# Performance work log

Measured on AMD Instinct MI355X. Metric: run time of the kernel, lower is better.

## Reference

```python
import jax, jax.numpy as jnp
import numpy as np

ST_HIDDEN = 128
ST_HEADS = 4
ST_LAYERS = 3
RES_SCALE = 1.0
DK = ST_HIDDEN // ST_HEADS


def build_3d_adj(spatial_ei, spatial_ea, n_nodes, window):
    # replicate spatial edges per time slice with node offset t*n_nodes
    offs = (jnp.arange(window) * n_nodes)[None, :, None]  # [1,W,1]
    all_sp_idx = (spatial_ei[:, None, :] + offs).reshape(2, -1)  # [2, W*E]
    all_sp_attr = jnp.tile(spatial_ea, (window, 1))  # [W*E, De]
    # temporal edges t -> t+1 for every node
    src = jnp.arange((window - 1) * n_nodes)
    temp_idx = jnp.stack([src, src + n_nodes], axis=0)  # [2, (W-1)*N]
    temp_attr = jnp.broadcast_to(spatial_ea.mean(axis=0, keepdims=True),
                                 (temp_idx.shape[1], spatial_ea.shape[1]))
    ei = jnp.concatenate([all_sp_idx, temp_idx], axis=1)
    ea = jnp.concatenate([all_sp_attr, temp_attr], axis=0)
    return ei, ea


def seg_softmax(logits, dst, num_nodes):
    # logits [E,H], segment softmax over dst (pyg_softmax)
    m = jax.ops.segment_max(logits, dst, num_segments=num_nodes)  # [N,H]
    ex = jnp.exp(logits - m[dst])
    s = jax.ops.segment_sum(ex, dst, num_segments=num_nodes)
    return ex / (s[dst] + 1e-16)


def layernorm(x, g, b, eps=1e-5):
    mu = x.mean(-1, keepdims=True)
    var = ((x - mu) ** 2).mean(-1, keepdims=True)
    return (x - mu) * jax.lax.rsqrt(var + eps) * g + b


def block(x, ei, ea, qw, qb, kw, kb, vw, vb, fw, fb, ow, ob, ln_g, ln_b):
    B, Nt, _ = x.shape
    H, dk = ST_HEADS, DK
    Q = (x @ qw + qb).reshape(B, Nt, H, dk)
    K = (x @ kw + kb).reshape(B, Nt, H, dk)
    V = (x @ vw + vb).reshape(B, Nt, H, dk)
    src, dst = ei[0], ei[1]
    q_e = Q[:, dst]  # [B,E,H,dk]
    k_e = K[:, src]
    v_e = V[:, src]
    film = ea @ fw + fb  # [E, 2*hidden]
    gamma, beta = jnp.split(film, 2, axis=-1)
    gamma = gamma.reshape(1, -1, H, dk)
    beta = beta.reshape(1, -1, H, dk)
    k_e = k_e * (1.0 + gamma) + beta
    logits = (q_e * k_e).sum(-1) / np.sqrt(dk).astype(np.float32)  # [B,E,H]
    att = jax.vmap(lambda l: seg_softmax(l, dst, Nt))(logits)
    msg = att[..., None] * v_e  # [B,E,H,dk]
    out = jnp.zeros((B, Nt, H, dk), x.dtype).at[:, dst].add(msg)
    y = out.reshape(B, Nt, H * dk) @ ow + ob
    return layernorm(x + y, ln_g, ln_b)


def setup_inputs() -> dict:
    key = jax.random.key(0)
    ks = jax.random.split(key, 12)
    B, W, N, Fin, E, De = 2, 16, 1000, 16, 16000, 8
    H, L = ST_HIDDEN, ST_LAYERS
    g = lambda k, s: jax.random.normal(k, s, jnp.float32) * 0.05
    return {
        "xw": jax.random.normal(ks[0], (B, W, N, Fin), jnp.float32),
        "spatial_ei": jax.random.randint(ks[1], (2, E), 0, N),
        "spatial_ea": jax.random.normal(ks[2], (E, De), jnp.float32),
        "in_w": g(ks[3], (Fin, H)), "in_b": jnp.zeros((H,), jnp.float32),
        "qw": g(ks[4], (L, H, H)), "qb": jnp.zeros((L, H), jnp.float32),
        "kw": g(ks[5], (L, H, H)), "kb": jnp.zeros((L, H), jnp.float32),
        "vw": g(ks[6], (L, H, H)), "vb": jnp.zeros((L, H), jnp.float32),
        "fw": g(ks[7], (L, De, 2 * H)), "fb": jnp.zeros((L, 2 * H), jnp.float32),
        "ow": g(ks[8], (L, H, H)), "ob": jnp.zeros((L, H), jnp.float32),
        "ln_g": jnp.ones((L, H), jnp.float32), "ln_b": jnp.zeros((L, H), jnp.float32),
        "head_w": g(ks[9], (H, 1)), "head_b": jnp.zeros((1,), jnp.float32),
    }


def reference(xw, spatial_ei, spatial_ea, in_w, in_b, qw, qb, kw, kb, vw, vb,
              fw, fb, ow, ob, ln_g, ln_b, head_w, head_b):
    B, W, N, Fin = xw.shape
    ei, ea = build_3d_adj(spatial_ei, spatial_ea, N, W)
    x = xw.reshape(B, W * N, Fin) @ in_w + in_b
    for l in range(ST_LAYERS):
        bx = block(x, ei, ea, qw[l], qb[l], kw[l], kb[l], vw[l], vb[l],
                   fw[l], fb[l], ow[l], ob[l], ln_g[l], ln_b[l])
        x = x + RES_SCALE * (bx - x)
    last = x.reshape(B, W, N, -1)[:, -1]  # [B,N,H]
    return jax.nn.softplus(last @ head_w + head_b).squeeze(-1)  # [B,N]
```

## Files before the change

### kernel.cpp

```cpp
#include <hip/hip_runtime.h>
#include <math.h>

constexpr int B    = 2;
constexpr int W    = 16;
constexpr int N    = 1000;
constexpr int FIN  = 16;
constexpr int E    = 16000;
constexpr int DE   = 8;
constexpr int H    = 128;
constexpr int L    = 3;
constexpr int WL   = 4;
constexpr int W0G  = 12;
constexpr int RPB  = WL * N;
constexpr int ROWS = B * RPB;
constexpr int NMAT = 12;

__device__ __forceinline__ float blockSum128(float v) {
  #pragma unroll
  for (int off = 32; off >= 1; off >>= 1) v += __shfl_xor(v, off);
  __shared__ float s2[2];
  int w = threadIdx.x >> 6;
  __syncthreads();
  if ((threadIdx.x & 63) == 0) s2[w] = v;
  __syncthreads();
  return s2[0] + s2[1];
}

__device__ __forceinline__ float dpp_add_xor1(float x) {
  int y = __builtin_amdgcn_update_dpp(0, __float_as_int(x), 0xB1, 0xF, 0xF, true);
  return x + __int_as_float(y);
}
__device__ __forceinline__ float dpp_add_xor2(float x) {
  int y = __builtin_amdgcn_update_dpp(0, __float_as_int(x), 0x4E, 0xF, 0xF, true);
  return x + __int_as_float(y);
}
__device__ __forceinline__ float headSum32(float p) {
  p = dpp_add_xor1(p);
  p = dpp_add_xor2(p);
  p += __shfl_xor(p, 4);
  p += __shfl_xor(p, 8);
  p += __shfl_xor(p, 16);
  return p;
}
__device__ __forceinline__ float dot4(float4 a, float4 b) {
  return a.x * b.x + a.y * b.y + a.z * b.z + a.w * b.w;
}

__global__ void k_count_scan(const int* __restrict__ ei, int* __restrict__ offs,
                             int* __restrict__ cursor, float* __restrict__ meanea) {
  __shared__ int cnt[N];
  __shared__ int scn[1024];
  int t = threadIdx.x;
  if (t < 8) meanea[t] = 0.f;
  if (t < N) cnt[t] = 0;
  __syncthreads();
  int vals[16];
  int nv = 0;
  for (int e = t; e < E; e += 1024) vals[nv++] = ei[E + e];
  for (int i = 0; i < nv; i++) atomicAdd(&cnt[vals[i]], 1);
  __syncthreads();
  int v = (t < N) ? cnt[t] : 0;
  scn[t] = v;
  __syncthreads();
  for (int st = 1; st < 1024; st <<= 1) {
    int add = (t >= st) ? scn[t - st] : 0;
    __syncthreads();
    scn[t] += add;
    __syncthreads();
  }
  if (t < N) {
    offs[t + 1] = scn[t];
    if (t == 0) offs[0] = 0;
    cursor[t] = scn[t] - v;
  }
}

__global__ void k_prep2(const int* __restrict__ ei, const float* __restrict__ ea,
                        int* __restrict__ cursor, int2* __restrict__ csr,
                        float* __restrict__ meanea,
                        const float* __restrict__ qw, const float* __restrict__ kw,
                        const float* __restrict__ vw, const float* __restrict__ ow,
                        float4* __restrict__ wTp4,
                        const float* __restrict__ xw, const float* __restrict__ in_w,
                        const float* __restrict__ in_b, float* __restrict__ x) {
  int bid = blockIdx.x;
  int t = threadIdx.x;
  if (bid < 64) {
    int e = bid * 256 + t;
    if (e < E) {
      int src = ei[e];
      int dst = ei[E + e];
      int pos = atomicAdd(&cursor[dst], 1);
      csr[pos] = make_int2(src, e);
    }
  } else if (bid < 128) {
    __shared__ float sbuf[256];
    int d = t & 7, g = t >> 3;
    float s = 0.f;
    for (int e = (bid - 64) * 32 + g; e < E; e += 64 * 32) s += ea[e * DE + d];
    sbuf[t] = s;
    __syncthreads();
    for (int st = 16; st >= 1; st >>= 1) {
      if (g < st) sbuf[g * 8 + d] += sbuf[(g + st) * 8 + d];
      __syncthreads();
    }
    if (g == 0) atomicAdd(&meanea[d], sbuf[d]);
  } else if (bid < 128 + NMAT * 16) {
    int bid2 = bid - 128;
    int mat = bid2 / 16;
    int pair = bid2 % 16;
    int kk4 = pair * 2 + (t >> 7);
    int c = t & 127;
    int l = mat >> 2, mm = mat & 3;
    const float* src = ((mm == 0) ? qw : (mm == 1) ? kw : (mm == 2) ? vw : ow) + (long)l * H * H;
    int k0 = kk4 * 4;
    float4 v4;
    v4.x = src[(k0 + 0) * H + c];
    v4.y = src[(k0 + 1) * H + c];
    v4.z = src[(k0 + 2) * H + c];
    v4.w = src[(k0 + 3) * H + c];
    wTp4[((long)mat * 32 + kk4) * H + c] = v4;
  } else {
    int bi = bid - (128 + NMAT * 16);
    int b = bi / 63, tt = bi % 63;
    int lr0 = tt * 64;
    __shared__ float xwS[64][FIN];
    __shared__ float inS[FIN][H];
    for (int i = t; i < 64 * FIN; i += 256) {
      int r = i >> 4, k = i & 15;
      int lr = lr0 + r;
      float val = 0.f;
      if (lr < RPB) {
        int wl = lr / N, n = lr % N;
        val = xw[(((long)b * W + (W0G + wl)) * N + n) * FIN + k];
      }
      xwS[r][k] = val;
    }
    for (int i = t; i < FIN * H; i += 256) inS[i >> 7][i & 127] = in_w[i];
    __syncthreads();
    #pragma unroll
    for (int qi = 0; qi < 8; qi++) {
      int idx = t + qi * 256;
      int r = idx >> 5, cq = idx & 31;
      int lr = lr0 + r;
      if (lr < RPB) {
        float4 acc = *(const float4*)(in_b + cq * 4);
        #pragma unroll
        for (int k = 0; k < FIN; k++) {
          float xv = xwS[r][k];
          float4 w4 = *(const float4*)(&inS[k][cq * 4]);
          acc.x += xv * w4.x; acc.y += xv * w4.y; acc.z += xv * w4.z; acc.w += xv * w4.w;
        }
        *(float4*)(x + ((long)b * RPB + lr) * H + cq * 4) = acc;
      }
    }
  }
}

__global__ void k_film(const float* __restrict__ ea, const float* __restrict__ fw,
                       const float* __restrict__ fb, const float* __restrict__ meanea,
                       unsigned int* __restrict__ filmh) {
  int e0 = blockIdx.x * 4;
  int t = threadIdx.x;
  float rgw[DE], rbw[DE];
  #pragma unroll
  for (int d = 0; d < DE; d++) {
    rgw[d] = fw[d * 2 * H + t];
    rbw[d] = fw[d * 2 * H + H + t];
  }
  float fbg = fb[t], fbb = fb[H + t];
  for (int e = e0; e < e0 + 4 && e <= E; e++) {
    float a[DE];
    if (e < E) {
      float4 a0 = *(const float4*)(ea + (long)e * DE);
      float4 a1 = *(const float4*)(ea + (long)e * DE + 4);
      a[0] = a0.x; a[1] = a0.y; a[2] = a0.z; a[3] = a0.w;
      a[4] = a1.x; a[5] = a1.y; a[6] = a1.z; a[7] = a1.w;
    } else {
      #pragma unroll
      for (int d = 0; d < DE; d++) a[d] = meanea[d] * (1.0f / E);
    }
    float g = fbg, be = fbb;
    #pragma unroll
    for (int d = 0; d < DE; d++) {
      g  += a[d] * rgw[d];
      be += a[d] * rbw[d];
    }
    unsigned int gb = __float_as_uint(g);
    gb = (gb + 0x7fffu + ((gb >> 16) & 1u)) >> 16;
    unsigned int bb_ = __float_as_uint(be);
    bb_ = (bb_ + 0x7fffu + ((bb_ >> 16) & 1u)) & 0xffff0000u;
    filmh[(long)e * H + t] = gb | bb_;
  }
}

__global__ void k_gemm(const float* __restrict__ X, const float4* __restrict__ wTp4,
                       int matBase,
                       const float* __restrict__ bq, const float* __restrict__ bk,
                       const float* __restrict__ bv,
                       float* __restrict__ Cq, float* __restrict__ Ck, float* __restrict__ Cv,
                       int base, int rows_pb, int tiles) {
  int m = blockIdx.y;
  const float* bm = (m == 0) ? bq : (m == 1) ? bk : bv;
  float* Cm       = (m == 0) ? Cq : (m == 1) ? Ck : Cv;
  const float4* wp = wTp4 + (long)(matBase + m) * 32 * H;
  int bb = blockIdx.x / tiles;
  int tt = blockIdx.x % tiles;
  int lr0 = tt * 32;
  long grow0 = (long)bb * RPB + base + lr0;
  int t = threadIdx.x;
  __shared__ float xs[32][H];
  #pragma unroll
  for (int qi = 0; qi < 4; qi++) {
    int idx = t + qi * 256;
    int r = idx >> 5, c4 = idx & 31;
    float4 v4 = make_float4(0.f, 0.f, 0.f, 0.f);
    if (lr0 + r < rows_pb) v4 = *(const float4*)(X + (grow0 + r) * H + c4 * 4);
    *(float4*)&xs[r][c4 * 4] = v4;
  }
  __syncthreads();
  int cg = t & 31, rg = t >> 5;
  float4 bias4 = *(const float4*)(bm + cg * 4);
  float4 acc0 = bias4, acc1 = bias4, acc2 = bias4, acc3 = bias4;
  #pragma unroll 4
  for (int kk4 = 0; kk4 < 32; kk4++) {
    const float4* wr = wp + kk4 * H + cg * 4;
    float4 w0 = wr[0], w1 = wr[1], w2 = wr[2], w3 = wr[3];
    float4 x0 = *(const float4*)&xs[rg * 4 + 0][kk4 * 4];
    float4 x1 = *(const float4*)&xs[rg * 4 + 1][kk4 * 4];
    float4 x2 = *(const float4*)&xs[rg * 4 + 2][kk4 * 4];
    float4 x3 = *(const float4*)&xs[rg * 4 + 3][kk4 * 4];
    acc0.x += dot4(x0, w0); acc0.y += dot4(x0, w1); acc0.z += dot4(x0, w2); acc0.w += dot4(x0, w3);
    acc1.x += dot4(x1, w0); acc1.y += dot4(x1, w1); acc1.z += dot4(x1, w2); acc1.w += dot4(x1, w3);
    acc2.x += dot4(x2, w0); acc2.y += dot4(x2, w1); acc2.z += dot4(x2, w2); acc2.w += dot4(x2, w3);
    acc3.x += dot4(x3, w0); acc3.y += dot4(x3, w1); acc3.z += dot4(x3, w2); acc3.w += dot4(x3, w3);
  }
  int lrr = lr0 + rg * 4;
  if (lrr + 0 < rows_pb) *(float4*)(Cm + (grow0 + rg * 4 + 0) * H + cg * 4) = acc0;
  if (lrr + 1 < rows_pb) *(float4*)(Cm + (grow0 + rg * 4 + 1) * H + cg * 4) = acc1;
  if (lrr + 2 < rows_pb) *(float4*)(Cm + (grow0 + rg * 4 + 2) * H + cg * 4) = acc2;
  if (lrr + 3 < rows_pb) *(float4*)(Cm + (grow0 + rg * 4 + 3) * H + cg * 4) = acc3;
}

__global__ void k_attn_oln(const float* __restrict__ Qb, const float* __restrict__ Kb,
                           const float* __restrict__ Vb,
                           const unsigned int* __restrict__ filmh,
                           const int* __restrict__ offs, const int2* __restrict__ csr,
                           const float* __restrict__ x, const float4* __restrict__ owp,
                           const float* __restrict__ ob, const float* __restrict__ lng,
                           const float* __restrict__ lnb, float* __restrict__ xo,
                           int out_lo,
                           const float* __restrict__ hw, const float* __restrict__ hb,
                           float* __restrict__ out, int do_head) {
  int tid = threadIdx.x;
  int nwin = WL - out_lo;
  int idx = blockIdx.x;
  int b = idx / (nwin * N);
  int rem = idx % (nwin * N);
  int wl = out_lo + rem / N;
  int n = rem % N;
  long drow = ((long)b * WL + wl) * N + n;
  float q = Qb[drow * H + tid];
  long sbase = ((long)b * WL + wl) * N;
  long trow  = ((long)b * WL + wl - 1) * N + n;
  const float scale = 0.17677669529663687f;
  int i0 = offs[n], i1 = offs[n + 1];

  unsigned int fh = filmh[(long)E * H + tid];
  float g  = __uint_as_float(fh << 16);
  float be = __uint_as_float(fh & 0xffff0000u);
  float kv = Kb[trow * H + tid];
  float vv = Vb[trow * H + tid];
  float p  = q * (kv * (1.f + g) + be);
  float pe = __expf(headSum32(p) * scale);
  float ssum = pe, acc = pe * vv;

  for (int i4 = i0; i4 < i1; i4 += 4) {
    #pragma unroll
    for (int j = 0; j < 4; j++) {
      int i = i4 + j;
      int ic = (i < i1) ? i : (i1 - 1);
      int2 se = csr[ic];
      long srow = sbase + se.x;
      unsigned int f2 = filmh[(long)se.y * H + tid];
      float g2 = __uint_as_float(f2 << 16);
      float b2 = __uint_as_float(f2 & 0xffff0000u);
      float kv2 = Kb[srow * H + tid];
      float vv2 = Vb[srow * H + tid];
      float p2  = q * (kv2 * (1.f + g2) + b2);
      float pe2 = __expf(headSum32(p2) * scale);
      pe2 = (i < i1) ? pe2 : 0.f;
      ssum += pe2;
      acc  += pe2 * vv2;
    }
  }
  float ab = acc / (ssum + 1e-16f);

  __shared__ float sab[H];
  sab[tid] = ab;
  __syncthreads();
  float y = ob[tid];
  #pragma unroll 8
  for (int kk4 = 0; kk4 < 32; kk4++) {
    float4 w4 = owp[kk4 * H + tid];
    float4 a4 = *(const float4*)&sab[kk4 * 4];
    y += dot4(a4, w4);
  }

  float v = x[drow * H + tid] + y;
  float mu = blockSum128(v) * (1.f / H);
  float dv = v - mu;
  float var = blockSum128(dv * dv) * (1.f / H);
  float o = dv * rsqrtf(var + 1e-5f) * lng[tid] + lnb[tid];

  if (!do_head) {
    xo[drow * H + tid] = o;
  } else {
    float hv = o * hw[tid];
    float tot = blockSum128(hv);
    if (tid == 0) {
      float z = tot + hb[0];
      out[b * N + n] = fmaxf(z, 0.f) + log1pf(expf(-fabsf(z)));
    }
  }
}

extern "C" void kernel_launch(void* const* d_in, const int* in_sizes, int n_in,
                              void* d_out, int out_size, void* d_ws, size_t ws_size,
                              hipStream_t stream) {
  const float* xw   = (const float*)d_in[0];
  const int*   ei   = (const int*)d_in[1];
  const float* ea   = (const float*)d_in[2];
  const float* in_w = (const float*)d_in[3];
  const float* in_b = (const float*)d_in[4];
  const float* qw   = (const float*)d_in[5];
  const float* qb   = (const float*)d_in[6];
  const float* kw   = (const float*)d_in[7];
  const float* kb   = (const float*)d_in[8];
  const float* vw   = (const float*)d_in[9];
  const float* vb   = (const float*)d_in[10];
  const float* fw   = (const float*)d_in[11];
  const float* fb   = (const float*)d_in[12];
  const float* ow   = (const float*)d_in[13];
  const float* ob   = (const float*)d_in[14];
  const float* ln_g = (const float*)d_in[15];
  const float* ln_b = (const float*)d_in[16];
  const float* hw   = (const float*)d_in[17];
  const float* hb   = (const float*)d_in[18];
  float* out = (float*)d_out;

  float* ws   = (float*)d_ws;
  float* x    = ws;
  float* x2   = x  + (long)ROWS * H;
  float* Qb   = x2 + (long)ROWS * H;
  float* Kb   = Qb + (long)ROWS * H;
  float* Vb   = Kb + (long)ROWS * H;
  float* wTp  = Vb + (long)ROWS * H;
  unsigned int* filmh = (unsigned int*)(wTp + (long)NMAT * H * H);
  float* meanea = (float*)(filmh + (long)(E + 1) * H);
  int* offs    = (int*)(meanea + 8);
  int* cursor  = offs + N + 1;
  int2* csr    = (int2*)(cursor + N);
  float4* wTp4 = (float4*)wTp;

  k_count_scan<<<1, 1024, 0, stream>>>(ei, offs, cursor, meanea);
  k_prep2<<<128 + NMAT * 16 + 126, 256, 0, stream>>>(
      ei, ea, cursor, csr, meanea, qw, kw, vw, ow, wTp4, xw, in_w, in_b, x);

  float* xa = x;
  float* xb = x2;
  for (int l = 0; l < L; l++) {
    int in_lo = l, out_lo = l + 1;
    k_film<<<(E + 1 + 3) / 4, 128, 0, stream>>>(
        ea, fw + (long)l * DE * 2 * H, fb + (long)l * 2 * H, meanea, filmh);
    int rows_pb = (WL - in_lo) * N;
    int tiles = (rows_pb + 31) / 32;
    k_gemm<<<dim3(B * tiles, 3), 256, 0, stream>>>(
        xa, wTp4, l * 4, qb + (long)l * H, kb + (long)l * H, vb + (long)l * H,
        Qb, Kb, Vb, in_lo * N, rows_pb, tiles);
    int nout = B * (WL - out_lo) * N;
    int last = (l == L - 1) ? 1 : 0;
    k_attn_oln<<<nout, H, 0, stream>>>(
        Qb, Kb, Vb, filmh, offs, csr,
        xa, wTp4 + ((long)l * 4 + 3) * 32 * H, ob + (long)l * H,
        ln_g + (long)l * H, ln_b + (long)l * H, xb, out_lo,
        hw, hb, out, last);
    float* tmp = xa; xa = xb; xb = tmp;
  }
}
```

Measured before the change: 263.5 us.

## Merge prep, film, gemm and CSR fill kernels; pack two nodes per attention block

Folds the count/scan into the prep kernel. Moves FiLM computation and CSR scatter into a combined mid kernel with the QKV GEMM, which cuts the launches per layer from three to two. The attention kernel now handles two destination nodes per 256-thread block, with per-half LayerNorm reductions in shared memory. The CSR fill now runs only in the layer-0 mid kernel, which adds ordering reliance on the prep kernel's cursor. The one-block scan now covers 4 counts per thread.

```diff
diff --git a/kernel.cpp b/kernel.cpp
--- a/kernel.cpp
+++ b/kernel.cpp
@@ -14,18 +14,11 @@
 constexpr int RPB  = WL * N;
 constexpr int ROWS = B * RPB;
 constexpr int NMAT = 12;
-
-__device__ __forceinline__ float blockSum128(float v) {
-  #pragma unroll
-  for (int off = 32; off >= 1; off >>= 1) v += __shfl_xor(v, off);
-  __shared__ float s2[2];
-  int w = threadIdx.x >> 6;
-  __syncthreads();
-  if ((threadIdx.x & 63) == 0) s2[w] = v;
-  __syncthreads();
-  return s2[0] + s2[1];
-}
-
+constexpr int NFILM = (E + 1 + 7) / 8;
+
+__device__ __forceinline__ float dot4(float4 a, float4 b) {
+  return a.x * b.x + a.y * b.y + a.z * b.z + a.w * b.w;
+}
 __device__ __forceinline__ float dpp_add_xor1(float x) {
   int y = __builtin_amdgcn_update_dpp(0, __float_as_int(x), 0xB1, 0xF, 0xF, true);
   return x + __int_as_float(y);
@@ -42,90 +35,89 @@
   p += __shfl_xor(p, 16);
   return p;
 }
-__device__ __forceinline__ float dot4(float4 a, float4 b) {
-  return a.x * b.x + a.y * b.y + a.z * b.z + a.w * b.w;
-}
-
-__global__ void k_count_scan(const int* __restrict__ ei, int* __restrict__ offs,
-                             int* __restrict__ cursor, float* __restrict__ meanea) {
-  __shared__ int cnt[N];
-  __shared__ int scn[1024];
-  int t = threadIdx.x;
-  if (t < 8) meanea[t] = 0.f;
-  if (t < N) cnt[t] = 0;
-  __syncthreads();
-  int vals[16];
-  int nv = 0;
-  for (int e = t; e < E; e += 1024) vals[nv++] = ei[E + e];
-  for (int i = 0; i < nv; i++) atomicAdd(&cnt[vals[i]], 1);
-  __syncthreads();
-  int v = (t < N) ? cnt[t] : 0;
-  scn[t] = v;
-  __syncthreads();
-  for (int st = 1; st < 1024; st <<= 1) {
-    int add = (t >= st) ? scn[t - st] : 0;
-    __syncthreads();
-    scn[t] += add;
-    __syncthreads();
-  }
-  if (t < N) {
-    offs[t + 1] = scn[t];
-    if (t == 0) offs[0] = 0;
-    cursor[t] = scn[t] - v;
-  }
-}
-
-__global__ void k_prep2(const int* __restrict__ ei, const float* __restrict__ ea,
-                        int* __restrict__ cursor, int2* __restrict__ csr,
-                        float* __restrict__ meanea,
-                        const float* __restrict__ qw, const float* __restrict__ kw,
-                        const float* __restrict__ vw, const float* __restrict__ ow,
-                        float4* __restrict__ wTp4,
-                        const float* __restrict__ xw, const float* __restrict__ in_w,
-                        const float* __restrict__ in_b, float* __restrict__ x) {
+
+__global__ void k_prep(const int* __restrict__ ei, const float* __restrict__ ea,
+                       const float* __restrict__ qw, const float* __restrict__ kw,
+                       const float* __restrict__ vw, const float* __restrict__ ow,
+                       float4* __restrict__ wTp4,
+                       const float* __restrict__ xw, const float* __restrict__ in_w,
+                       const float* __restrict__ in_b, float* __restrict__ x,
+                       float* __restrict__ meanea, int* __restrict__ offs,
+                       int* __restrict__ cursor) {
+  __shared__ union {
+    struct { int cnt[1024]; int sT[256]; } sc;
+    struct { float xwS[64][FIN]; float inS[FIN][H]; } ip;
+    float sbuf[256];
+  } sm;
   int bid = blockIdx.x;
   int t = threadIdx.x;
-  if (bid < 64) {
-    int e = bid * 256 + t;
-    if (e < E) {
-      int src = ei[e];
-      int dst = ei[E + e];
-      int pos = atomicAdd(&cursor[dst], 1);
-      csr[pos] = make_int2(src, e);
-    }
-  } else if (bid < 128) {
-    __shared__ float sbuf[256];
+  if (bid == 0) {
+    int* cnt = sm.sc.cnt;
+    for (int i = t; i < 1024; i += 256) cnt[i] = 0;
+    __syncthreads();
+    for (int e0 = t; e0 < E; e0 += 1024) {
+      int v[4];
+      #pragma unroll
+      for (int j = 0; j < 4; j++) {
+        int e = e0 + j * 256;
+        v[j] = (e < E) ? ei[E + e] : -1;
+      }
+      #pragma unroll
+      for (int j = 0; j < 4; j++) if (v[j] >= 0) atomicAdd(&cnt[v[j]], 1);
+    }
+    __syncthreads();
+    int idx0 = t * 4;
+    int c0 = cnt[idx0], c1 = cnt[idx0 + 1], c2 = cnt[idx0 + 2], c3 = cnt[idx0 + 3];
+    int run = c0 + c1 + c2 + c3;
+    int* sT = sm.sc.sT;
+    sT[t] = run;
+    __syncthreads();
+    for (int st = 1; st < 256; st <<= 1) {
+      int add = (t >= st) ? sT[t - st] : 0;
+      __syncthreads();
+      sT[t] += add;
+      __syncthreads();
+    }
+    int pos = sT[t] - run;
+    int cs[4] = {c0, c1, c2, c3};
+    #pragma unroll
+    for (int j = 0; j < 4; j++) {
+      int i = idx0 + j;
+      if (i < N) { offs[i + 1] = pos + cs[j]; cursor[i] = pos; }
+      pos += cs[j];
+    }
+    if (t == 0) offs[0] = 0;
+  } else if (bid < 49) {
+    int u0 = (bid - 1) * 1024;
+    #pragma unroll
+    for (int q = 0; q < 4; q++) {
+      int o = u0 + q * 256 + t;
+      int mat = o >> 12, rem = o & 4095;
+      int kk4 = rem >> 7, c = rem & 127;
+      int l = mat >> 2, mm = mat & 3;
+      const float* src = ((mm == 0) ? qw : (mm == 1) ? kw : (mm == 2) ? vw : ow)
+                         + (long)l * H * H;
+      int k0 = kk4 * 4;
+      float4 v4 = make_float4(src[(k0 + 0) * H + c], src[(k0 + 1) * H + c],
+                              src[(k0 + 2) * H + c], src[(k0 + 3) * H + c]);
+      wTp4[o] = v4;
+    }
+  } else if (bid < 81) {
+    int eb = bid - 49;
     int d = t & 7, g = t >> 3;
     float s = 0.f;
-    for (int e = (bid - 64) * 32 + g; e < E; e += 64 * 32) s += ea[e * DE + d];
-    sbuf[t] = s;
+    for (int e = eb * 32 + g; e < E; e += 32 * 32) s += ea[e * DE + d];
+    sm.sbuf[t] = s;
     __syncthreads();
     for (int st = 16; st >= 1; st >>= 1) {
-      if (g < st) sbuf[g * 8 + d] += sbuf[(g + st) * 8 + d];
+      if (g < st) sm.sbuf[g * 8 + d] += sm.sbuf[(g + st) * 8 + d];
       __syncthreads();
     }
-    if (g == 0) atomicAdd(&meanea[d], sbuf[d]);
-  } else if (bid < 128 + NMAT * 16) {
-    int bid2 = bid - 128;
-    int mat = bid2 / 16;
-    int pair = bid2 % 16;
-    int kk4 = pair * 2 + (t >> 7);
-    int c = t & 127;
-    int l = mat >> 2, mm = mat & 3;
-    const float* src = ((mm == 0) ? qw : (mm == 1) ? kw : (mm == 2) ? vw : ow) + (long)l * H * H;
-    int k0 = kk4 * 4;
-    float4 v4;
-    v4.x = src[(k0 + 0) * H + c];
-    v4.y = src[(k0 + 1) * H + c];
-    v4.z = src[(k0 + 2) * H + c];
-    v4.w = src[(k0 + 3) * H + c];
-    wTp4[((long)mat * 32 + kk4) * H + c] = v4;
+    if (g == 0) atomicAdd(&meanea[d], sm.sbuf[d]);
   } else {
-    int bi = bid - (128 + NMAT * 16);
+    int bi = bid - 81;
     int b = bi / 63, tt = bi % 63;
     int lr0 = tt * 64;
-    __shared__ float xwS[64][FIN];
-    __shared__ float inS[FIN][H];
     for (int i = t; i < 64 * FIN; i += 256) {
       int r = i >> 4, k = i & 15;
       int lr = lr0 + r;
@@ -134,9 +126,9 @@
         int wl = lr / N, n = lr % N;
         val = xw[(((long)b * W + (W0G + wl)) * N + n) * FIN + k];
       }
-      xwS[r][k] = val;
-    }
-    for (int i = t; i < FIN * H; i += 256) inS[i >> 7][i & 127] = in_w[i];
+      sm.ip.xwS[r][k] = val;
+    }
+    for (int i = t; i < FIN * H; i += 256) sm.ip.inS[i >> 7][i & 127] = in_w[i];
     __syncthreads();
     #pragma unroll
     for (int qi = 0; qi < 8; qi++) {
@@ -147,8 +139,8 @@
         float4 acc = *(const float4*)(in_b + cq * 4);
         #pragma unroll
         for (int k = 0; k < FIN; k++) {
-          float xv = xwS[r][k];
-          float4 w4 = *(const float4*)(&inS[k][cq * 4]);
+          float xv = sm.ip.xwS[r][k];
+          float4 w4 = *(const float4*)(&sm.ip.inS[k][cq * 4]);
           acc.x += xv * w4.x; acc.y += xv * w4.y; acc.z += xv * w4.z; acc.w += xv * w4.w;
         }
         *(float4*)(x + ((long)b * RPB + lr) * H + cq * 4) = acc;
@@ -157,89 +149,104 @@
   }
 }
 
-__global__ void k_film(const float* __restrict__ ea, const float* __restrict__ fw,
-                       const float* __restrict__ fb, const float* __restrict__ meanea,
-                       unsigned int* __restrict__ filmh) {
-  int e0 = blockIdx.x * 4;
+__global__ void k_mid(const float* __restrict__ X, const float4* __restrict__ wTp4,
+                      int matBase,
+                      const float* __restrict__ bq, const float* __restrict__ bk,
+                      const float* __restrict__ bv,
+                      float* __restrict__ Cq, float* __restrict__ Ck, float* __restrict__ Cv,
+                      int base, int rows_pb, int tiles, int nG,
+                      const float* __restrict__ ea, const float* __restrict__ fwl,
+                      const float* __restrict__ fbl, const float* __restrict__ meanea,
+                      unsigned int* __restrict__ filmh,
+                      const int* __restrict__ ei, int* __restrict__ cursor,
+                      int2* __restrict__ csr) {
+  __shared__ float xs[32][H];
+  int u = blockIdx.x;
   int t = threadIdx.x;
-  float rgw[DE], rbw[DE];
-  #pragma unroll
-  for (int d = 0; d < DE; d++) {
-    rgw[d] = fw[d * 2 * H + t];
-    rbw[d] = fw[d * 2 * H + H + t];
-  }
-  float fbg = fb[t], fbb = fb[H + t];
-  for (int e = e0; e < e0 + 4 && e <= E; e++) {
-    float a[DE];
+  if (u < nG) {
+    int m = u / (B * tiles);
+    int r2 = u % (B * tiles);
+    int bb = r2 / tiles, tt = r2 % tiles;
+    const float* bm = (m == 0) ? bq : (m == 1) ? bk : bv;
+    float* Cm       = (m == 0) ? Cq : (m == 1) ? Ck : Cv;
+    const float4* wp = wTp4 + (long)(matBase + m) * 32 * H;
+    int lr0 = tt * 32;
+    long grow0 = (long)bb * RPB + base + lr0;
+    #pragma unroll
+    for (int qi = 0; qi < 4; qi++) {
+      int idx = t + qi * 256;
+      int r = idx >> 5, c4 = idx & 31;
+      float4 v4 = make_float4(0.f, 0.f, 0.f, 0.f);
+      if (lr0 + r < rows_pb) v4 = *(const float4*)(X + (grow0 + r) * H + c4 * 4);
+      *(float4*)&xs[r][c4 * 4] = v4;
+    }
+    __syncthreads();
+    int cg = t & 31, rg = t >> 5;
+    float4 bias4 = *(const float4*)(bm + cg * 4);
+    float4 acc0 = bias4, acc1 = bias4, acc2 = bias4, acc3 = bias4;
+    #pragma unroll 4
+    for (int kk4 = 0; kk4 < 32; kk4++) {
+      const float4* wr = wp + kk4 * H + cg * 4;
+      float4 w0 = wr[0], w1 = wr[1], w2 = wr[2], w3 = wr[3];
+      float4 x0 = *(const float4*)&xs[rg * 4 + 0][kk4 * 4];
+      float4 x1 = *(const float4*)&xs[rg * 4 + 1][kk4 * 4];
+      float4 x2 = *(const float4*)&xs[rg * 4 + 2][kk4 * 4];
+      float4 x3 = *(const float4*)&xs[rg * 4 + 3][kk4 * 4];
+      acc0.x += dot4(x0, w0); acc0.y += dot4(x0, w1); acc0.z += dot4(x0, w2); acc0.w += dot4(x0, w3);
+      acc1.x += dot4(x1, w0); acc1.y += dot4(x1, w1); acc1.z += dot4(x1, w2); acc1.w += dot4(x1, w3);
+      acc2.x += dot4(x2, w0); acc2.y += dot4(x2, w1); acc2.z += dot4(x2, w2); acc2.w += dot4(x2, w3);
+      acc3.x += dot4(x3, w0); acc3.y += dot4(x3, w1); acc3.z += dot4(x3, w2); acc3.w += dot4(x3, w3);
+    }
+    int lrr = lr0 + rg * 4;
+    if (lrr + 0 < rows_pb) *(float4*)(Cm + (grow0 + rg * 4 + 0) * H + cg * 4) = acc0;
+    if (lrr + 1 < rows_pb) *(float4*)(Cm + (grow0 + rg * 4 + 1) * H + cg * 4) = acc1;
+    if (lrr + 2 < rows_pb) *(float4*)(Cm + (grow0 + rg * 4 + 2) * H + cg * 4) = acc2;
+    if (lrr + 3 < rows_pb) *(float4*)(Cm + (grow0 + rg * 4 + 3) * H + cg * 4) = acc3;
+  } else if (u < nG + NFILM) {
+    int ru = u - nG;
+    int c = t & 127, g2 = t >> 7;
+    float rgw[DE], rbw[DE];
+    #pragma unroll
+    for (int d = 0; d < DE; d++) {
+      rgw[d] = fwl[d * 2 * H + c];
+      rbw[d] = fwl[d * 2 * H + H + c];
+    }
+    float fbg = fbl[c], fbb = fbl[H + c];
+    int e0 = ru * 8 + g2 * 4;
+    for (int e = e0; e < e0 + 4; e++) {
+      if (e > E) break;
+      float a[DE];
+      if (e < E) {
+        float4 a0 = *(const float4*)(ea + (long)e * DE);
+        float4 a1 = *(const float4*)(ea + (long)e * DE + 4);
+        a[0] = a0.x; a[1] = a0.y; a[2] = a0.z; a[3] = a0.w;
+        a[4] = a1.x; a[5] = a1.y; a[6] = a1.z; a[7] = a1.w;
+      } else {
+        #pragma unroll
+        for (int d = 0; d < DE; d++) a[d] = meanea[d] * (1.0f / E);
+      }
+      float g = fbg, be = fbb;
+      #pragma unroll
+      for (int d = 0; d < DE; d++) {
+        g  += a[d] * rgw[d];
+        be += a[d] * rbw[d];
+      }
+      unsigned int gb = __float_as_uint(g);
+      gb = (gb + 0x7fffu + ((gb >> 16) & 1u)) >> 16;
+      unsigned int bb_ = __float_as_uint(be);
+      bb_ = (bb_ + 0x7fffu + ((bb_ >> 16) & 1u)) & 0xffff0000u;
+      filmh[(long)e * H + c] = gb | bb_;
+    }
+  } else {
+    int f = u - nG - NFILM;
+    int e = f * 256 + t;
     if (e < E) {
-      float4 a0 = *(const float4*)(ea + (long)e * DE);
-      float4 a1 = *(const float4*)(ea + (long)e * DE + 4);
-      a[0] = a0.x; a[1] = a0.y; a[2] = a0.z; a[3] = a0.w;
-      a[4] = a1.x; a[5] = a1.y; a[6] = a1.z; a[7] = a1.w;
-    } else {
-      #pragma unroll
-      for (int d = 0; d < DE; d++) a[d] = meanea[d] * (1.0f / E);
-    }
-    float g = fbg, be = fbb;
-    #pragma unroll
-    for (int d = 0; d < DE; d++) {
-      g  += a[d] * rgw[d];
-      be += a[d] * rbw[d];
-    }
-    unsigned int gb = __float_as_uint(g);
-    gb = (gb + 0x7fffu + ((gb >> 16) & 1u)) >> 16;
-    unsigned int bb_ = __float_as_uint(be);
-    bb_ = (bb_ + 0x7fffu + ((bb_ >> 16) & 1u)) & 0xffff0000u;
-    filmh[(long)e * H + t] = gb | bb_;
-  }
-}
-
-__global__ void k_gemm(const float* __restrict__ X, const float4* __restrict__ wTp4,
-                       int matBase,
-                       const float* __restrict__ bq, const float* __restrict__ bk,
-                       const float* __restrict__ bv,
-                       float* __restrict__ Cq, float* __restrict__ Ck, float* __restrict__ Cv,
-                       int base, int rows_pb, int tiles) {
-  int m = blockIdx.y;
-  const float* bm = (m == 0) ? bq : (m == 1) ? bk : bv;
-  float* Cm       = (m == 0) ? Cq : (m == 1) ? Ck : Cv;
-  const float4* wp = wTp4 + (long)(matBase + m) * 32 * H;
-  int bb = blockIdx.x / tiles;
-  int tt = blockIdx.x % tiles;
-  int lr0 = tt * 32;
-  long grow0 = (long)bb * RPB + base + lr0;
-  int t = threadIdx.x;
-  __shared__ float xs[32][H];
-  #pragma unroll
-  for (int qi = 0; qi < 4; qi++) {
-    int idx = t + qi * 256;
-    int r = idx >> 5, c4 = idx & 31;
-    float4 v4 = make_float4(0.f, 0.f, 0.f, 0.f);
-    if (lr0 + r < rows_pb) v4 = *(const float4*)(X + (grow0 + r) * H + c4 * 4);
-    *(float4*)&xs[r][c4 * 4] = v4;
-  }
-  __syncthreads();
-  int cg = t & 31, rg = t >> 5;
-  float4 bias4 = *(const float4*)(bm + cg * 4);
-  float4 acc0 = bias4, acc1 = bias4, acc2 = bias4, acc3 = bias4;
-  #pragma unroll 4
-  for (int kk4 = 0; kk4 < 32; kk4++) {
-    const float4* wr = wp + kk4 * H + cg * 4;
-    float4 w0 = wr[0], w1 = wr[1], w2 = wr[2], w3 = wr[3];
-    float4 x0 = *(const float4*)&xs[rg * 4 + 0][kk4 * 4];
-    float4 x1 = *(const float4*)&xs[rg * 4 + 1][kk4 * 4];
-    float4 x2 = *(const float4*)&xs[rg * 4 + 2][kk4 * 4];
-    float4 x3 = *(const float4*)&xs[rg * 4 + 3][kk4 * 4];
-    acc0.x += dot4(x0, w0); acc0.y += dot4(x0, w1); acc0.z += dot4(x0, w2); acc0.w += dot4(x0, w3);
-    acc1.x += dot4(x1, w0); acc1.y += dot4(x1, w1); acc1.z += dot4(x1, w2); acc1.w += dot4(x1, w3);
-    acc2.x += dot4(x2, w0); acc2.y += dot4(x2, w1); acc2.z += dot4(x2, w2); acc2.w += dot4(x2, w3);
-    acc3.x += dot4(x3, w0); acc3.y += dot4(x3, w1); acc3.z += dot4(x3, w2); acc3.w += dot4(x3, w3);
-  }
-  int lrr = lr0 + rg * 4;
-  if (lrr + 0 < rows_pb) *(float4*)(Cm + (grow0 + rg * 4 + 0) * H + cg * 4) = acc0;
-  if (lrr + 1 < rows_pb) *(float4*)(Cm + (grow0 + rg * 4 + 1) * H + cg * 4) = acc1;
-  if (lrr + 2 < rows_pb) *(float4*)(Cm + (grow0 + rg * 4 + 2) * H + cg * 4) = acc2;
-  if (lrr + 3 < rows_pb) *(float4*)(Cm + (grow0 + rg * 4 + 3) * H + cg * 4) = acc3;
+      int src = ei[e];
+      int dst = ei[E + e];
+      int pos = atomicAdd(&cursor[dst], 1);
+      csr[pos] = make_int2(src, e);
+    }
+  }
 }
 
 __global__ void k_attn_oln(const float* __restrict__ Qb, const float* __restrict__ Kb,
@@ -252,9 +259,12 @@
                            int out_lo,
                            const float* __restrict__ hw, const float* __restrict__ hb,
                            float* __restrict__ out, int do_head) {
-  int tid = threadIdx.x;
+  __shared__ float sab[2][H];
+  __shared__ float red[2][2];
+  int t = threadIdx.x;
+  int half = t >> 7, tid = t & 127;
+  int idx = blockIdx.x * 2 + half;
   int nwin = WL - out_lo;
-  int idx = blockIdx.x;
   int b = idx / (nwin * N);
   int rem = idx % (nwin * N);
   int wl = out_lo + rem / N;
@@ -271,8 +281,8 @@
   float be = __uint_as_float(fh & 0xffff0000u);
   float kv = Kb[trow * H + tid];
   float vv = Vb[trow * H + tid];
-  float p  = q * (kv * (1.f + g) + be);
-  float pe = __expf(headSum32(p) * scale);
+  float pp = q * (kv * (1.f + g) + be);
+  float pe = __expf(headSum32(pp) * scale);
   float ssum = pe, acc = pe * vv;
 
   for (int i4 = i0; i4 < i1; i4 += 4) {
@@ -296,30 +306,56 @@
   }
   float ab = acc / (ssum + 1e-16f);
 
-  __shared__ float sab[H];
-  sab[tid] = ab;
+  sab[half][tid] = ab;
   __syncthreads();
   float y = ob[tid];
   #pragma unroll 8
   for (int kk4 = 0; kk4 < 32; kk4++) {
     float4 w4 = owp[kk4 * H + tid];
-    float4 a4 = *(const float4*)&sab[kk4 * 4];
+    float4 a4 = *(const float4*)&sab[half][kk4 * 4];
     y += dot4(a4, w4);
   }
 
   float v = x[drow * H + tid] + y;
-  float mu = blockSum128(v) * (1.f / H);
-  float dv = v - mu;
-  float var = blockSum128(dv * dv) * (1.f / H);
+  #pragma unroll
+  for (int off = 32; off >= 1; off >>= 1) v += 0.f;
+  float s = x[drow * H + tid] + y;
+  float r1 = s;
+  #pragma unroll
+  for (int off = 32; off >= 1; off >>= 1) r1 += __shfl_xor(r1, off);
+  {
+    int w = (t >> 6) & 1;
+    __syncthreads();
+    if ((t & 63) == 0) red[half][w] = r1;
+    __syncthreads();
+  }
+  float mu = (red[half][0] + red[half][1]) * (1.f / H);
+  float dv = s - mu;
+  float r2v = dv * dv;
+  #pragma unroll
+  for (int off = 32; off >= 1; off >>= 1) r2v += __shfl_xor(r2v, off);
+  {
+    int w = (t >> 6) & 1;
+    __syncthreads();
+    if ((t & 63) == 0) red[half][w] = r2v;
+    __syncthreads();
+  }
+  float var = (red[half][0] + red[half][1]) * (1.f / H);
   float o = dv * rsqrtf(var + 1e-5f) * lng[tid] + lnb[tid];
 
   if (!do_head) {
     xo[drow * H + tid] = o;
   } else {
     float hv = o * hw[tid];
-    float tot = blockSum128(hv);
+    float r3 = hv;
+    #pragma unroll
+    for (int off = 32; off >= 1; off >>= 1) r3 += __shfl_xor(r3, off);
+    int w = (t >> 6) & 1;
+    __syncthreads();
+    if ((t & 63) == 0) red[half][w] = r3;
+    __syncthreads();
     if (tid == 0) {
-      float z = tot + hb[0];
+      float z = red[half][0] + red[half][1] + hb[0];
       out[b * N + n] = fmaxf(z, 0.f) + log1pf(expf(-fabsf(z)));
     }
   }
@@ -363,24 +399,27 @@
   int2* csr    = (int2*)(cursor + N);
   float4* wTp4 = (float4*)wTp;
 
-  k_count_scan<<<1, 1024, 0, stream>>>(ei, offs, cursor, meanea);
-  k_prep2<<<128 + NMAT * 16 + 126, 256, 0, stream>>>(
-      ei, ea, cursor, csr, meanea, qw, kw, vw, ow, wTp4, xw, in_w, in_b, x);
+  hipMemsetAsync(meanea, 0, 8 * sizeof(float), stream);
+  k_prep<<<207, 256, 0, stream>>>(ei, ea, qw, kw, vw, ow, wTp4,
+                                  xw, in_w, in_b, x, meanea, offs, cursor);
 
   float* xa = x;
   float* xb = x2;
   for (int l = 0; l < L; l++) {
-    int in_lo = l, out_lo = l + 1;
-    k_film<<<(E + 1 + 3) / 4, 128, 0, stream>>>(
-        ea, fw + (long)l * DE * 2 * H, fb + (long)l * 2 * H, meanea, filmh);
-    int rows_pb = (WL - in_lo) * N;
+    int out_lo = l + 1;
+    int rows_pb = (WL - l) * N;
     int tiles = (rows_pb + 31) / 32;
-    k_gemm<<<dim3(B * tiles, 3), 256, 0, stream>>>(
+    int nG = 3 * B * tiles;
+    int nFill = (l == 0) ? (E + 255) / 256 : 0;
+    int nMid = nG + NFILM + nFill;
+    k_mid<<<nMid, 256, 0, stream>>>(
         xa, wTp4, l * 4, qb + (long)l * H, kb + (long)l * H, vb + (long)l * H,
-        Qb, Kb, Vb, in_lo * N, rows_pb, tiles);
+        Qb, Kb, Vb, l * N, rows_pb, tiles, nG,
+        ea, fw + (long)l * DE * 2 * H, fb + (long)l * 2 * H, meanea, filmh,
+        ei, cursor, csr);
     int nout = B * (WL - out_lo) * N;
     int last = (l == L - 1) ? 1 : 0;
-    k_attn_oln<<<nout, H, 0, stream>>>(
+    k_attn_oln<<<nout / 2, 256, 0, stream>>>(
         Qb, Kb, Vb, filmh, offs, csr,
         xa, wTp4 + ((long)l * 4 + 3) * 32 * H, ob + (long)l * H,
         ln_g + (long)l * H, ln_b + (long)l * H, xb, out_lo,
```

Measured after the change: 269.1 us. +2.1%, slower.
